# Kernel optimization log

Measured on AMD Instinct MI355X. Metric: run time of the kernel, lower is better.

The kernel has to match this reference:

```python
import jax, jax.numpy as jnp
import numpy as np

N_NODES = 50000
N_EDGES = 800000
IN_DIM = 128
IN_CH = 64
HIDDEN = 64
OUT_CH = 128
NUM_CLS = 16
NUM_GRAPHS = 512


def setup_inputs() -> dict:
    key = jax.random.key(0)
    ks = jax.random.split(key, 16)
    s = 0.02
    x = jax.random.normal(ks[0], (N_NODES, IN_DIM), jnp.float32)
    edge_index = jax.random.randint(ks[1], (2, N_EDGES), 0, N_NODES, jnp.int64)
    batch = jnp.sort(jax.random.randint(ks[2], (N_NODES,), 0, NUM_GRAPHS, jnp.int64))
    return {
        "x": x,
        "edge_index": edge_index,
        "batch": batch,
        "num_graphs": NUM_GRAPHS,
        "w_stage1": jax.random.normal(ks[3], (IN_DIM, IN_CH), jnp.float32) * s,
        "b_stage1": jnp.zeros((IN_CH,), jnp.float32),
        "rel1_w": jax.random.normal(ks[4], (IN_CH, HIDDEN), jnp.float32) * s,
        "rel1_b": jnp.zeros((HIDDEN,), jnp.float32),
        "root1_w": jax.random.normal(ks[5], (IN_CH, HIDDEN), jnp.float32) * s,
        "rel2_w": jax.random.normal(ks[6], (HIDDEN, 2 * HIDDEN), jnp.float32) * s,
        "rel2_b": jnp.zeros((2 * HIDDEN,), jnp.float32),
        "root2_w": jax.random.normal(ks[7], (HIDDEN, 2 * HIDDEN), jnp.float32) * s,
        "rel3_w": jax.random.normal(ks[8], (2 * HIDDEN, OUT_CH), jnp.float32) * s,
        "rel3_b": jnp.zeros((OUT_CH,), jnp.float32),
        "root3_w": jax.random.normal(ks[9], (2 * HIDDEN, OUT_CH), jnp.float32) * s,
        "lin_w": jax.random.normal(ks[10], (OUT_CH, NUM_CLS), jnp.float32) * s,
        "lin_b": jnp.zeros((NUM_CLS,), jnp.float32),
    }


def graph_conv(x, src, dst, rel_w, rel_b, root_w, n_nodes):
    # PyG GraphConv(aggr='add'): lin_rel(sum_{j in N(i)} x_j) + lin_root(x_i)
    agg = jax.ops.segment_sum(x[src], dst, num_segments=n_nodes)  # [N, in]
    return agg @ rel_w + rel_b + x @ root_w


def reference(x, edge_index, batch, num_graphs,
              w_stage1, b_stage1,
              rel1_w, rel1_b, root1_w,
              rel2_w, rel2_b, root2_w,
              rel3_w, rel3_b, root3_w,
              lin_w, lin_b):
    src, dst = edge_index[0], edge_index[1]
    n = x.shape[0]
    h = x @ w_stage1 + b_stage1                                   # [N, IN_CH]
    h = jax.nn.relu(graph_conv(h, src, dst, rel1_w, rel1_b, root1_w, n))
    h = jax.nn.relu(graph_conv(h, src, dst, rel2_w, rel2_b, root2_w, n))
    h = jax.nn.relu(graph_conv(h, src, dst, rel3_w, rel3_b, root3_w, n))
    # global mean pool over graphs
    sums = jax.ops.segment_sum(h, batch, num_segments=num_graphs)  # [G, OUT_CH]
    cnt = jax.ops.segment_sum(jnp.ones((n,), h.dtype), batch, num_segments=num_graphs)
    pooled = sums / jnp.maximum(cnt, 1.0)[:, None]
    # dropout treated as identity (deterministic eval reference)
    return pooled @ lin_w + lin_b                                  # [G, NUM_CLS]
```

## Files before the change

kernel.cpp:

```cpp
#include <hip/hip_runtime.h>
#include <hip/hip_bf16.h>

#define N_NODES 50000
#define N_EDGES 800000
#define IN_DIM  128
#define IN_CH   64
#define HIDDEN  64
#define OUT_CH  128
#define NUM_CLS 16
#define NUM_G   512
#define NBUK    ((N_NODES + 255) >> 8)
#define BCAP    6144
#define EPB_A   4096

typedef __attribute__((ext_vector_type(8))) short short8;
typedef __attribute__((ext_vector_type(4))) float f32x4;

__device__ inline float bits2f(unsigned short u) {
  unsigned x = (unsigned)u << 16;
  float f;
  __builtin_memcpy(&f, &x, 4);
  return f;
}
__device__ inline unsigned short f2bits(float v) {
  __hip_bfloat16 b = __float2bfloat16(v);
  unsigned short s;
  __builtin_memcpy(&s, &b, 2);
  return s;
}
__device__ inline short8 zero8() {
  short8 z;
#pragma unroll
  for (int i = 0; i < 8; ++i) z[i] = 0;
  return z;
}
__device__ inline void acc2(float& a0, float& a1, unsigned v) {
  a0 += bits2f((unsigned short)v);
  a1 += bits2f((unsigned short)(v >> 16));
}
__device__ inline void accu4(float* a, uint4 v) {
  acc2(a[0], a[1], v.x); acc2(a[2], a[3], v.y);
  acc2(a[4], a[5], v.z); acc2(a[6], a[7], v.w);
}

__global__ __launch_bounds__(64) void k_stage1(
    const float* __restrict__ Ap, const short* __restrict__ Wa,
    const float* __restrict__ bias, unsigned short* __restrict__ outp) {
  constexpr int DIN = 128, DOUT = 64, KT = DIN / 32, CT = DOUT / 16;
  const int lane = threadIdx.x;
  const int m = lane & 15;
  const int q = lane >> 4;
  const int row = blockIdx.x * 16 + m;
  const bool ok = row < N_NODES;

  short8 afr[KT];
#pragma unroll
  for (int kt = 0; kt < KT; ++kt) {
    short8 f = zero8();
    if (ok) {
      const float* ap = Ap + (size_t)row * DIN + kt * 32 + q * 8;
      float4 x0 = *(const float4*)ap;
      float4 x1 = *(const float4*)(ap + 4);
      f[0] = (short)f2bits(x0.x); f[1] = (short)f2bits(x0.y);
      f[2] = (short)f2bits(x0.z); f[3] = (short)f2bits(x0.w);
      f[4] = (short)f2bits(x1.x); f[5] = (short)f2bits(x1.y);
      f[6] = (short)f2bits(x1.z); f[7] = (short)f2bits(x1.w);
    }
    afr[kt] = f;
  }
  const int rbase = blockIdx.x * 16;
#pragma unroll
  for (int ct = 0; ct < CT; ++ct) {
    f32x4 c = {0.f, 0.f, 0.f, 0.f};
#pragma unroll
    for (int kt = 0; kt < KT; ++kt) {
      short8 b = *(const short8*)(Wa + ((size_t)(kt * CT + ct) * 64 + lane) * 8);
      c = __builtin_amdgcn_mfma_f32_16x16x32_bf16(afr[kt], b, c, 0, 0, 0);
    }
    float bv = bias[ct * 16 + m];
#pragma unroll
    for (int r = 0; r < 4; ++r) {
      int ro = rbase + q * 4 + r;
      if (ro < N_NODES) outp[(size_t)ro * DOUT + ct * 16 + m] = f2bits(c[r] + bv);
    }
  }
}

template <int DIN, int DOUT>
__global__ __launch_bounds__(256) void k_fused(
    const unsigned short* __restrict__ h, const int* __restrict__ esrc,
    const int* __restrict__ off, const short* __restrict__ Wa,
    const short* __restrict__ Wh, const float* __restrict__ bias,
    unsigned short* __restrict__ outp) {
  constexpr int KT = DIN / 32;
  constexpr int CT = DOUT / 16;
  constexpr int NE = KT * 8;
  __shared__ float lsum[3 * NE * 64];

  const int tid = threadIdx.x;
  const int wave = tid >> 6;
  const int lane = tid & 63;
  const int m = lane & 15;
  const int q = lane >> 4;
  const int node = blockIdx.x * 16 + m;

  float acc[KT][8];
#pragma unroll
  for (int kt = 0; kt < KT; ++kt)
#pragma unroll
    for (int j = 0; j < 8; ++j) acc[kt][j] = 0.f;

  if (node < N_NODES) {
    int beg = off[node], len = off[node + 1] - beg;
    int e = beg + (len * wave) / 4;
    int end = beg + (len * (wave + 1)) / 4;
    const unsigned short* hq = h + q * 8;
    for (; e + 2 <= end; e += 2) {
      int s0 = esrc[e], s1 = esrc[e + 1];
      const unsigned short* r0 = hq + (size_t)s0 * DIN;
      const unsigned short* r1 = hq + (size_t)s1 * DIN;
#pragma unroll
      for (int kt = 0; kt < KT; ++kt) {
        uint4 va = *(const uint4*)(r0 + kt * 32);
        uint4 vb = *(const uint4*)(r1 + kt * 32);
        accu4(acc[kt], va);
        accu4(acc[kt], vb);
      }
    }
    if (e < end) {
      const unsigned short* r0 = hq + (size_t)esrc[e] * DIN;
#pragma unroll
      for (int kt = 0; kt < KT; ++kt)
        accu4(acc[kt], *(const uint4*)(r0 + kt * 32));
    }
  }

  if (wave > 0) {
    float* base = lsum + (size_t)(wave - 1) * NE * 64 + lane;
#pragma unroll
    for (int kt = 0; kt < KT; ++kt)
#pragma unroll
      for (int j = 0; j < 8; ++j) base[(kt * 8 + j) * 64] = acc[kt][j];
  }
  __syncthreads();
  if (wave != 0) return;

#pragma unroll
  for (int w = 0; w < 3; ++w) {
    const float* base = lsum + (size_t)w * NE * 64 + lane;
#pragma unroll
    for (int kt = 0; kt < KT; ++kt)
#pragma unroll
      for (int j = 0; j < 8; ++j) acc[kt][j] += base[(kt * 8 + j) * 64];
  }

  short8 afr[KT], hfr[KT];
#pragma unroll
  for (int kt = 0; kt < KT; ++kt) {
    short8 f;
#pragma unroll
    for (int j = 0; j < 8; ++j) f[j] = (short)f2bits(acc[kt][j]);
    afr[kt] = f;
    hfr[kt] = (node < N_NODES)
                  ? *(const short8*)(h + (size_t)node * DIN + kt * 32 + q * 8)
                  : zero8();
  }

  const int rbase = blockIdx.x * 16;
#pragma unroll
  for (int ct = 0; ct < CT; ++ct) {
    f32x4 c = {0.f, 0.f, 0.f, 0.f};
#pragma unroll
    for (int kt = 0; kt < KT; ++kt) {
      short8 b = *(const short8*)(Wa + ((size_t)(kt * CT + ct) * 64 + lane) * 8);
      c = __builtin_amdgcn_mfma_f32_16x16x32_bf16(afr[kt], b, c, 0, 0, 0);
      short8 bh = *(const short8*)(Wh + ((size_t)(kt * CT + ct) * 64 + lane) * 8);
      c = __builtin_amdgcn_mfma_f32_16x16x32_bf16(hfr[kt], bh, c, 0, 0, 0);
    }
    float bv = bias[ct * 16 + m];
#pragma unroll
    for (int r = 0; r < 4; ++r) {
      int row = rbase + q * 4 + r;
      if (row < N_NODES)
        outp[(size_t)row * DOUT + ct * 16 + m] = f2bits(fmaxf(c[r] + bv, 0.f));
    }
  }
}

template <int DIN, int DOUT>
__device__ inline void pack1(const float* __restrict__ W, short* __restrict__ o,
                             int t) {
  constexpr int CT = DOUT / 16;
  int j = t & 7;
  int lane = (t >> 3) & 63;
  int kc = t >> 9;
  int ct = kc % CT;
  int kt = kc / CT;
  int k = kt * 32 + (lane >> 4) * 8 + j;
  int n = ct * 16 + (lane & 15);
  o[t] = (short)f2bits(W[k * DOUT + n]);
}

__global__ __launch_bounds__(256) void k_packall(
    const float* w1, const float* r1, const float* o1, const float* r2,
    const float* o2, const float* r3, const float* o3,
    short* w1p, short* r1p, short* o1p, short* r2p, short* o2p,
    short* r3p, short* o3p) {
  int b = blockIdx.x, t = threadIdx.x;
  if      (b < 32)  pack1<128, 64>(w1, w1p, (b - 0) * 256 + t);
  else if (b < 48)  pack1<64, 64>(r1, r1p, (b - 32) * 256 + t);
  else if (b < 64)  pack1<64, 64>(o1, o1p, (b - 48) * 256 + t);
  else if (b < 96)  pack1<64, 128>(r2, r2p, (b - 64) * 256 + t);
  else if (b < 128) pack1<64, 128>(o2, o2p, (b - 96) * 256 + t);
  else if (b < 192) pack1<128, 128>(r3, r3p, (b - 128) * 256 + t);
  else              pack1<128, 128>(o3, o3p, (b - 192) * 256 + t);
}

__global__ __launch_bounds__(256) void k_bucketA(const int* __restrict__ src,
    const int* __restrict__ dst, int* __restrict__ bcnt, uint2* __restrict__ bbuf) {
  __shared__ int hist[NBUK], sbase[NBUK], lcur[NBUK];
  const int t = threadIdx.x;
  for (int i = t; i < NBUK; i += 256) { hist[i] = 0; lcur[i] = 0; }
  __syncthreads();
  const int e0 = blockIdx.x * EPB_A;
  int s_[16], d_[16];
  int cnt = 0;
#pragma unroll
  for (int k = 0; k < 16; ++k) {
    int e = e0 + k * 256 + t;
    if (e < N_EDGES) {
      s_[cnt] = src[e]; d_[cnt] = dst[e];
      atomicAdd(&hist[d_[cnt] >> 8], 1);
      cnt++;
    }
  }
  __syncthreads();
  for (int i = t; i < NBUK; i += 256) sbase[i] = atomicAdd(&bcnt[i], hist[i]);
  __syncthreads();
  for (int k = 0; k < cnt; ++k) {
    int b = d_[k] >> 8;
    int pos = sbase[b] + atomicAdd(&lcur[b], 1);
    if (pos < BCAP) bbuf[(size_t)b * BCAP + pos] = make_uint2((unsigned)s_[k], (unsigned)d_[k]);
  }
}

__global__ __launch_bounds__(256) void k_scanb(const int* __restrict__ bcnt,
    int* __restrict__ bbase, int* __restrict__ off) {
  __shared__ int s[256];
  int t = threadIdx.x;
  int v0 = (t < NBUK) ? min(bcnt[t], BCAP) : 0;
  s[t] = v0;
  __syncthreads();
  for (int st = 1; st < 256; st <<= 1) {
    int v = (t >= st) ? s[t - st] : 0;
    __syncthreads();
    s[t] += v;
    __syncthreads();
  }
  if (t < NBUK) bbase[t] = s[t] - v0;
  if (t == NBUK - 1) off[N_NODES] = s[t];
}

__global__ __launch_bounds__(256) void k_bfin(const int* __restrict__ bcnt,
    const uint2* __restrict__ bbuf, const int* __restrict__ bbase,
    int* __restrict__ off, int* __restrict__ esrc) {
  __shared__ int cnt[256], s[256], soff[256];
  const int b = blockIdx.x;
  const int t = threadIdx.x;
  cnt[t] = 0;
  __syncthreads();
  int n = min(bcnt[b], BCAP);
  for (int i = t; i < n; i += 256)
    atomicAdd(&cnt[bbuf[(size_t)b * BCAP + i].y & 255], 1);
  __syncthreads();
  int v0 = cnt[t];
  s[t] = v0;
  __syncthreads();
  for (int st = 1; st < 256; st <<= 1) {
    int v = (t >= st) ? s[t - st] : 0;
    __syncthreads();
    s[t] += v;
    __syncthreads();
  }
  int myoff = bbase[b] + s[t] - v0;
  int node = b * 256 + t;
  if (node < N_NODES) off[node] = myoff;
  soff[t] = myoff;
  cnt[t] = 0;
  __syncthreads();
  for (int i = t; i < n; i += 256) {
    uint2 p = bbuf[(size_t)b * BCAP + i];
    int l = p.y & 255;
    int r = atomicAdd(&cnt[l], 1);
    esrc[soff[l] + r] = (int)p.x;
  }
}

__device__ inline int lbound(const int* __restrict__ a, int n, int v) {
  int lo = 0, hi = n;
  while (lo < hi) {
    int m = (lo + hi) >> 1;
    if (a[m] < v) lo = m + 1; else hi = m;
  }
  return lo;
}

__global__ __launch_bounds__(128) void k_poolhead(const unsigned short* __restrict__ h3,
    const int* __restrict__ batch, const float* __restrict__ lw,
    const float* __restrict__ lb, float* __restrict__ out) {
  __shared__ float sp[128];
  int g = blockIdx.x;
  int t = threadIdx.x;
  int lo = lbound(batch, N_NODES, g);
  int hi = lbound(batch, N_NODES, g + 1);
  float a0 = 0.f, a1 = 0.f, a2 = 0.f, a3 = 0.f;
  int r = lo;
  for (; r + 4 <= hi; r += 4) {
    a0 += bits2f(h3[(size_t)(r + 0) * OUT_CH + t]);
    a1 += bits2f(h3[(size_t)(r + 1) * OUT_CH + t]);
    a2 += bits2f(h3[(size_t)(r + 2) * OUT_CH + t]);
    a3 += bits2f(h3[(size_t)(r + 3) * OUT_CH + t]);
  }
  for (; r < hi; ++r) a0 += bits2f(h3[(size_t)r * OUT_CH + t]);
  float inv = (hi > lo) ? 1.f / (float)(hi - lo) : 0.f;
  sp[t] = ((a0 + a1) + (a2 + a3)) * inv;
  __syncthreads();
  if (t < NUM_CLS) {
    float s = lb[t];
#pragma unroll
    for (int k = 0; k < OUT_CH; ++k) s = fmaf(sp[k], lw[k * NUM_CLS + t], s);
    out[g * NUM_CLS + t] = s;
  }
}

extern "C" void kernel_launch(void* const* d_in, const int* in_sizes, int n_in,
                              void* d_out, int out_size, void* d_ws, size_t ws_size,
                              hipStream_t stream) {
  const float* x      = (const float*)d_in[0];
  const int*   ei     = (const int*)d_in[1];
  const int*   batch  = (const int*)d_in[2];
  const float* w1     = (const float*)d_in[4];
  const float* b1     = (const float*)d_in[5];
  const float* rel1w  = (const float*)d_in[6];
  const float* rel1b  = (const float*)d_in[7];
  const float* root1w = (const float*)d_in[8];
  const float* rel2w  = (const float*)d_in[9];
  const float* rel2b  = (const float*)d_in[10];
  const float* root2w = (const float*)d_in[11];
  const float* rel3w  = (const float*)d_in[12];
  const float* rel3b  = (const float*)d_in[13];
  const float* root3w = (const float*)d_in[14];
  const float* linw   = (const float*)d_in[15];
  const float* linb   = (const float*)d_in[16];
  const int* src = ei;
  const int* dst = ei + N_EDGES;
  float* out = (float*)d_out;

  unsigned short* P = (unsigned short*)d_ws;
  unsigned short* Q = P + (size_t)N_NODES * 128;
  unsigned short* R = Q + (size_t)N_NODES * 128;
  short* WP = (short*)(R + (size_t)N_NODES * 128);
  short* w1p  = WP;
  short* r1p  = w1p + 8192;
  short* o1p  = r1p + 4096;
  short* r2p  = o1p + 4096;
  short* o2p  = r2p + 8192;
  short* r3p  = o2p + 8192;
  short* o3p  = r3p + 16384;
  int* off     = (int*)(o3p + 16384);
  int* bcnt    = off + (N_NODES + 1);
  int* bbase   = bcnt + NBUK;
  int* esrc    = bbase + NBUK + 2;
  uint2* bbuf  = (uint2*)((char*)(esrc + N_EDGES) +
                          ((16 - (((size_t)(esrc + N_EDGES)) & 15)) & 15));

  hipMemsetAsync(bcnt, 0, NBUK * sizeof(int), stream);
  k_bucketA<<<(N_EDGES + EPB_A - 1) / EPB_A, 256, 0, stream>>>(src, dst, bcnt, bbuf);
  k_scanb<<<1, 256, 0, stream>>>(bcnt, bbase, off);
  k_bfin<<<NBUK, 256, 0, stream>>>(bcnt, bbuf, bbase, off, esrc);

  k_packall<<<256, 256, 0, stream>>>(w1, rel1w, root1w, rel2w, root2w, rel3w,
                                     root3w, w1p, r1p, o1p, r2p, o2p, r3p, o3p);

  const int GF = (N_NODES + 15) / 16;

  k_stage1<<<GF, 64, 0, stream>>>(x, w1p, b1, P);
  k_fused<64, 64><<<GF, 256, 0, stream>>>(P, esrc, off, r1p, o1p, rel1b, R);
  k_fused<64, 128><<<GF, 256, 0, stream>>>(R, esrc, off, r2p, o2p, rel2b, Q);
  k_fused<128, 128><<<GF, 256, 0, stream>>>(Q, esrc, off, r3p, o3p, rel3b, P);
  k_poolhead<<<NUM_G, 128, 0, stream>>>(P, batch, linw, linb, out);
}
```

Measured before the change: 283.1 us.

## Use one wave per 16-node tile with deeper unrolled edge gathers

Each fused GraphConv block now uses a single 64-lane wave instead of four waves that split each node's edge list and reduce partial sums through shared memory. Each lane walks its node's whole edge list with UN-way unrolled batches of independent row loads, giving more memory-level parallelism per lane. This removes the LDS reduction and the block barrier, and the self-row load is hoisted before the gather. The cost is less parallelism per node, longer serial loops for high-degree nodes, and higher register pressure from the unrolled load buffers.

Measured after the change: 264.3 us. 1.07x faster.

```diff
diff --git a/kernel.cpp b/kernel.cpp
--- a/kernel.cpp
+++ b/kernel.cpp
@@ -86,23 +86,25 @@
   }
 }
 
-template <int DIN, int DOUT>
-__global__ __launch_bounds__(256) void k_fused(
+template <int DIN, int DOUT, int UN>
+__global__ __launch_bounds__(64) void k_fused(
     const unsigned short* __restrict__ h, const int* __restrict__ esrc,
     const int* __restrict__ off, const short* __restrict__ Wa,
     const short* __restrict__ Wh, const float* __restrict__ bias,
     unsigned short* __restrict__ outp) {
   constexpr int KT = DIN / 32;
   constexpr int CT = DOUT / 16;
-  constexpr int NE = KT * 8;
-  __shared__ float lsum[3 * NE * 64];
-
-  const int tid = threadIdx.x;
-  const int wave = tid >> 6;
-  const int lane = tid & 63;
+  const int lane = threadIdx.x;
   const int m = lane & 15;
   const int q = lane >> 4;
   const int node = blockIdx.x * 16 + m;
+  const bool ok = node < N_NODES;
+
+  short8 hfr[KT];
+#pragma unroll
+  for (int kt = 0; kt < KT; ++kt)
+    hfr[kt] = ok ? *(const short8*)(h + (size_t)node * DIN + kt * 32 + q * 8)
+                 : zero8();
 
   float acc[KT][8];
 #pragma unroll
@@ -110,24 +112,27 @@
 #pragma unroll
     for (int j = 0; j < 8; ++j) acc[kt][j] = 0.f;
 
-  if (node < N_NODES) {
-    int beg = off[node], len = off[node + 1] - beg;
-    int e = beg + (len * wave) / 4;
-    int end = beg + (len * (wave + 1)) / 4;
+  if (ok) {
+    int e = off[node], end = off[node + 1];
     const unsigned short* hq = h + q * 8;
-    for (; e + 2 <= end; e += 2) {
-      int s0 = esrc[e], s1 = esrc[e + 1];
-      const unsigned short* r0 = hq + (size_t)s0 * DIN;
-      const unsigned short* r1 = hq + (size_t)s1 * DIN;
-#pragma unroll
-      for (int kt = 0; kt < KT; ++kt) {
-        uint4 va = *(const uint4*)(r0 + kt * 32);
-        uint4 vb = *(const uint4*)(r1 + kt * 32);
-        accu4(acc[kt], va);
-        accu4(acc[kt], vb);
+    int sv[UN];
+    uint4 tv[UN][KT];
+    for (; e + UN <= end; e += UN) {
+#pragma unroll
+      for (int u = 0; u < UN; ++u) sv[u] = esrc[e + u];
+#pragma unroll
+      for (int u = 0; u < UN; ++u) {
+        const unsigned short* r0 = hq + (size_t)sv[u] * DIN;
+#pragma unroll
+        for (int kt = 0; kt < KT; ++kt)
+          tv[u][kt] = *(const uint4*)(r0 + kt * 32);
       }
-    }
-    if (e < end) {
+#pragma unroll
+      for (int u = 0; u < UN; ++u)
+#pragma unroll
+        for (int kt = 0; kt < KT; ++kt) accu4(acc[kt], tv[u][kt]);
+    }
+    for (; e < end; ++e) {
       const unsigned short* r0 = hq + (size_t)esrc[e] * DIN;
 #pragma unroll
       for (int kt = 0; kt < KT; ++kt)
@@ -135,35 +140,13 @@
     }
   }
 
-  if (wave > 0) {
-    float* base = lsum + (size_t)(wave - 1) * NE * 64 + lane;
-#pragma unroll
-    for (int kt = 0; kt < KT; ++kt)
-#pragma unroll
-      for (int j = 0; j < 8; ++j) base[(kt * 8 + j) * 64] = acc[kt][j];
-  }
-  __syncthreads();
-  if (wave != 0) return;
-
-#pragma unroll
-  for (int w = 0; w < 3; ++w) {
-    const float* base = lsum + (size_t)w * NE * 64 + lane;
-#pragma unroll
-    for (int kt = 0; kt < KT; ++kt)
-#pragma unroll
-      for (int j = 0; j < 8; ++j) acc[kt][j] += base[(kt * 8 + j) * 64];
-  }
-
-  short8 afr[KT], hfr[KT];
+  short8 afr[KT];
 #pragma unroll
   for (int kt = 0; kt < KT; ++kt) {
     short8 f;
 #pragma unroll
     for (int j = 0; j < 8; ++j) f[j] = (short)f2bits(acc[kt][j]);
     afr[kt] = f;
-    hfr[kt] = (node < N_NODES)
-                  ? *(const short8*)(h + (size_t)node * DIN + kt * 32 + q * 8)
-                  : zero8();
   }
 
   const int rbase = blockIdx.x * 16;
@@ -385,8 +368,8 @@
   const int GF = (N_NODES + 15) / 16;
 
   k_stage1<<<GF, 64, 0, stream>>>(x, w1p, b1, P);
-  k_fused<64, 64><<<GF, 256, 0, stream>>>(P, esrc, off, r1p, o1p, rel1b, R);
-  k_fused<64, 128><<<GF, 256, 0, stream>>>(R, esrc, off, r2p, o2p, rel2b, Q);
-  k_fused<128, 128><<<GF, 256, 0, stream>>>(Q, esrc, off, r3p, o3p, rel3b, P);
+  k_fused<64, 64, 8><<<GF, 64, 0, stream>>>(P, esrc, off, r1p, o1p, rel1b, R);
+  k_fused<64, 128, 8><<<GF, 64, 0, stream>>>(R, esrc, off, r2p, o2p, rel2b, Q);
+  k_fused<128, 128, 4><<<GF, 64, 0, stream>>>(Q, esrc, off, r3p, o3p, rel3b, P);
   k_poolhead<<<NUM_G, 128, 0, stream>>>(P, batch, linw, linb, out);
 }
```
